# Kernel optimization log

Hardware: AMD Instinct MI355X
Metric: run time of the kernel (lower is better)

## Reference

```python
import jax, jax.numpy as jnp
import numpy as np

S = 14
B = 2
C = 20
LAMBDA_COORD = 5.0
LAMBDA_NOOBJ = 0.5
BATCH = 4096


def setup_inputs() -> dict:
    key = jax.random.key(0)
    k1, k2, k3 = jax.random.split(key, 3)
    pred = jax.random.uniform(k1, (BATCH, S, S, B * 5 + C), dtype=jnp.float32)
    target = jax.random.uniform(k2, (BATCH, S, S, B * 5 + C), dtype=jnp.float32)
    obj = (jax.random.uniform(k3, (BATCH, S, S), dtype=jnp.float32) < 0.15).astype(jnp.float32)
    target = target.at[..., 4].set(obj)
    target = target.at[..., 9].set(obj)
    return {"pred": pred, "target": target}


def _iou(box1, box2):
    # box1, box2: (..., 4) = [x, y, w, h]; elementwise IoU over leading dims
    b1x1 = box1[..., 0] - box1[..., 2] / 2
    b1y1 = box1[..., 1] - box1[..., 3] / 2
    b1x2 = box1[..., 0] + box1[..., 2] / 2
    b1y2 = box1[..., 1] + box1[..., 3] / 2
    b2x1 = box2[..., 0] - box2[..., 2] / 2
    b2y1 = box2[..., 1] - box2[..., 3] / 2
    b2x2 = box2[..., 0] + box2[..., 2] / 2
    b2y2 = box2[..., 1] + box2[..., 3] / 2
    iw = jnp.clip(jnp.minimum(b1x2, b2x2) - jnp.maximum(b1x1, b2x1), 0)
    ih = jnp.clip(jnp.minimum(b1y2, b2y2) - jnp.maximum(b1y1, b2y1), 0)
    inter = iw * ih
    a1 = (b1x2 - b1x1) * (b1y2 - b1y1)
    a2 = (b2x2 - b2x1) * (b2y2 - b2y1)
    return inter / (a1 + a2 - inter + 1e-6)


def reference(pred, target):
    bs = pred.shape[0]
    tb = target[..., : B * 5].reshape(bs, S, S, B, 5)
    pb = pred[..., : B * 5].reshape(bs, S, S, B, 5)
    tcls = target[..., B * 5 :]
    pcls = pred[..., B * 5 :]

    obj_mask = tb[..., 4] > 0          # (bs,S,S,B)
    has_obj = obj_mask[..., 0]         # (bs,S,S)
    noobj_mask = ~obj_mask

    # no-object confidence loss over every non-obj box slot
    conf_err2 = (pb[..., 4] - tb[..., 4]) ** 2
    noobj_loss = jnp.sum(jnp.where(noobj_mask, conf_err2, 0.0))

    # per-box IoU between i-th pred box and i-th target box in each cell
    ious = _iou(pb[..., :4], tb[..., :4])            # (bs,S,S,B)
    best_idx = jnp.argmax(ious, axis=-1)             # (bs,S,S)
    idx = best_idx[..., None, None]
    p_best = jnp.take_along_axis(pb, idx, axis=3)[..., 0, :]  # (bs,S,S,5)
    t_best = jnp.take_along_axis(tb, idx, axis=3)[..., 0, :]

    m = has_obj                                       # (bs,S,S) bool
    mf = m.astype(pred.dtype)

    xy_loss = jnp.sum(mf[..., None] * (p_best[..., :2] - t_best[..., :2]) ** 2)
    p_wh = jnp.sqrt(jnp.abs(p_best[..., 2:4]) + 1e-6)
    t_wh_safe = jnp.where(m[..., None], t_best[..., 2:4], 1.0)  # avoid sqrt(0) grad NaN
    t_wh = jnp.sqrt(t_wh_safe)
    wh_loss = jnp.sum(mf[..., None] * (p_wh - t_wh) ** 2)
    coord_loss = xy_loss + wh_loss

    obj_loss = jnp.sum(mf * (p_best[..., 4] - t_best[..., 4]) ** 2)

    # non-best box confidence pushed to 0 (B=2: the other slot)
    nonbest_conf = jnp.sum(pb[..., 4], axis=-1) - p_best[..., 4]
    noobj_loss = noobj_loss + LAMBDA_NOOBJ * jnp.sum(mf * nonbest_conf ** 2)

    class_loss = jnp.sum(mf[..., None] * (pcls - tcls) ** 2)

    total = LAMBDA_COORD * coord_loss + obj_loss + LAMBDA_NOOBJ * noobj_loss + class_loss
    return total / bs
```

## Files before the change

### kernel.cpp

```cpp
#include <hip/hip_runtime.h>


#define FEAT 30
#define CELLS 802816
#define TILE_CELLS 64
#define TILE_FLOATS (TILE_CELLS * FEAT)
#define BUF_FLOATS (2 * TILE_FLOATS)
#define TILES_PER_BLOCK 8
#define NB (CELLS / (TILE_CELLS * TILES_PER_BLOCK))

__device__ __forceinline__ void load16(const float* g, float* l) {
    __builtin_amdgcn_global_load_lds(
        (const __attribute__((address_space(1))) void*)g,
        (__attribute__((address_space(3))) void*)l, 16, 0, 0);
}

__device__ __forceinline__ float iou_f(float x1, float y1, float w1, float h1,
                                       float x2, float y2, float w2, float h2) {
    float b1x1 = x1 - 0.5f * w1, b1x2 = x1 + 0.5f * w1;
    float b1y1 = y1 - 0.5f * h1, b1y2 = y1 + 0.5f * h1;
    float b2x1 = x2 - 0.5f * w2, b2x2 = x2 + 0.5f * w2;
    float b2y1 = y2 - 0.5f * h2, b2y2 = y2 + 0.5f * h2;
    float iw = fmaxf(fminf(b1x2, b2x2) - fmaxf(b1x1, b2x1), 0.0f);
    float ih = fmaxf(fminf(b1y2, b2y2) - fmaxf(b1y1, b2y1), 0.0f);
    float inter = iw * ih;
    float a1 = (b1x2 - b1x1) * (b1y2 - b1y1);
    float a2 = (b2x2 - b2x1) * (b2y2 - b2y1);
    return inter / (a1 + a2 - inter + 1e-6f);
}

__device__ __forceinline__ float cell_loss(const float* p, const float* t) {
    const bool obj0 = t[4] > 0.0f;
    const bool obj1 = t[9] > 0.0f;
    const float mf = obj0 ? 1.0f : 0.0f;

    float d0 = p[4] - t[4];
    float d1 = p[9] - t[9];
    float noobj = (obj0 ? 0.0f : d0 * d0) + (obj1 ? 0.0f : d1 * d1);

    float iou0 = iou_f(p[0], p[1], p[2], p[3], t[0], t[1], t[2], t[3]);
    float iou1 = iou_f(p[5], p[6], p[7], p[8], t[5], t[6], t[7], t[8]);
    const bool sel1 = iou1 > iou0;

    float pbx = sel1 ? p[5] : p[0];
    float pby = sel1 ? p[6] : p[1];
    float pbw = sel1 ? p[7] : p[2];
    float pbh = sel1 ? p[8] : p[3];
    float pbc = sel1 ? p[9] : p[4];
    float tbx = sel1 ? t[5] : t[0];
    float tby = sel1 ? t[6] : t[1];
    float tbw = sel1 ? t[7] : t[2];
    float tbh = sel1 ? t[8] : t[3];
    float tbc = sel1 ? t[9] : t[4];

    float dx = pbx - tbx, dy = pby - tby;
    float xy = dx * dx + dy * dy;

    float pw = sqrtf(fabsf(pbw) + 1e-6f);
    float ph = sqrtf(fabsf(pbh) + 1e-6f);
    float tw = sqrtf(obj0 ? tbw : 1.0f);
    float th = sqrtf(obj0 ? tbh : 1.0f);
    float dw = pw - tw, dh = ph - th;
    float wh = dw * dw + dh * dh;

    float dc = pbc - tbc;
    float obj_l = dc * dc;

    float nonbest = (p[4] + p[9]) - pbc;
    noobj += 0.5f * mf * nonbest * nonbest;

    float cls = 0.0f;
#pragma unroll
    for (int k = 10; k < FEAT; ++k) {
        float d = p[k] - t[k];
        cls += d * d;
    }

    return 5.0f * mf * (xy + wh) + mf * obj_l + 0.5f * noobj + mf * cls;
}

__global__ __launch_bounds__(64, 2) void yolo_kernel(
        const float* __restrict__ pred, const float* __restrict__ tgt,
        float* __restrict__ out) {
    __shared__ float lds[2 * BUF_FLOATS];

    const int lane = threadIdx.x;
    const float* predT = pred + (long long)blockIdx.x * TILES_PER_BLOCK * TILE_FLOATS;
    const float* tgtT  = tgt  + (long long)blockIdx.x * TILES_PER_BLOCK * TILE_FLOATS;

    const float* pl = predT + lane * 4;
    const float* ml = (lane < 32) ? (predT + 1792 + lane * 4)
                                  : (tgtT - 128 + lane * 4);
    const float* tl = tgtT + 128 + lane * 4;

    auto stage = [&](int buf, int tileFloatOff) {
        float* L = lds + buf * BUF_FLOATS;
        const float* p = pl + tileFloatOff;
        const float* m = ml + tileFloatOff;
        const float* t = tl + tileFloatOff;
#pragma unroll
        for (int j = 0; j < 7; ++j) load16(p + j * 256, L + j * 256);
        load16(m, L + 1792);
#pragma unroll
        for (int j = 0; j < 7; ++j) load16(t + j * 256, L + 2048 + j * 256);
    };

    stage(0, 0);
    float acc = 0.0f;

#pragma unroll 1
    for (int i = 0; i < TILES_PER_BLOCK; ++i) {
        if (i + 1 < TILES_PER_BLOCK) stage((i + 1) & 1, (i + 1) * TILE_FLOATS);

        const float2* pc = (const float2*)(lds + (i & 1) * BUF_FLOATS + lane * FEAT);
        const float2* tc = (const float2*)(lds + (i & 1) * BUF_FLOATS + TILE_FLOATS + lane * FEAT);
        float pf[FEAT], tf[FEAT];
#pragma unroll
        for (int k = 0; k < FEAT / 2; ++k) {
            float2 a = pc[k]; pf[2 * k] = a.x; pf[2 * k + 1] = a.y;
            float2 b = tc[k]; tf[2 * k] = b.x; tf[2 * k + 1] = b.y;
        }
        acc += cell_loss(pf, tf);
    }

    float v = acc;
#pragma unroll
    for (int off = 32; off > 0; off >>= 1) v += __shfl_down(v, off, 64);
    if (lane == 0) atomicAdd(out, v * (1.0f / 4096.0f));
}

extern "C" void kernel_launch(void* const* d_in, const int* in_sizes, int n_in,
                              void* d_out, int out_size, void* d_ws, size_t ws_size,
                              hipStream_t stream) {
    const float* pred = (const float*)d_in[0];
    const float* tgt  = (const float*)d_in[1];
    float* out = (float*)d_out;

    hipMemsetAsync(out, 0, sizeof(float), stream);
    yolo_kernel<<<NB, 64, 0, stream>>>(pred, tgt, out);
}
```

Before: 215.2 us.

## Use one tile per block with partial sums and a separate reduction kernel

Each block now processes a single 64-cell tile, dropping the 8-tile double-buffered loop, so the grid holds 12544 single-wave blocks instead of 1568. Per-block sums go to a workspace array and a second single-block kernel reduces them, replacing the global atomicAdd and the memset. This aims for more memory-level parallelism and less atomic contention. The cost is an extra kernel launch, the loss of load/compute overlap inside a block, and a small serial reduction over 12544 partials.

```diff
diff --git a/kernel.cpp b/kernel.cpp
--- a/kernel.cpp
+++ b/kernel.cpp
@@ -5,9 +5,8 @@
 #define CELLS 802816
 #define TILE_CELLS 64
 #define TILE_FLOATS (TILE_CELLS * FEAT)
-#define BUF_FLOATS (2 * TILE_FLOATS)
-#define TILES_PER_BLOCK 8
-#define NB (CELLS / (TILE_CELLS * TILES_PER_BLOCK))
+#define NB (CELLS / TILE_CELLS)
+#define RED_TPB 256
 
 __device__ __forceinline__ void load16(const float* g, float* l) {
     __builtin_amdgcn_global_load_lds(
@@ -79,54 +78,56 @@
     return 5.0f * mf * (xy + wh) + mf * obj_l + 0.5f * noobj + mf * cls;
 }
 
-__global__ __launch_bounds__(64, 2) void yolo_kernel(
+__global__ __launch_bounds__(64) void yolo_kernel(
         const float* __restrict__ pred, const float* __restrict__ tgt,
-        float* __restrict__ out) {
-    __shared__ float lds[2 * BUF_FLOATS];
+        float* __restrict__ partials) {
+    __shared__ float lds[2 * TILE_FLOATS];
 
     const int lane = threadIdx.x;
-    const float* predT = pred + (long long)blockIdx.x * TILES_PER_BLOCK * TILE_FLOATS;
-    const float* tgtT  = tgt  + (long long)blockIdx.x * TILES_PER_BLOCK * TILE_FLOATS;
+    const float* predT = pred + (long long)blockIdx.x * TILE_FLOATS;
+    const float* tgtT  = tgt  + (long long)blockIdx.x * TILE_FLOATS;
 
     const float* pl = predT + lane * 4;
     const float* ml = (lane < 32) ? (predT + 1792 + lane * 4)
                                   : (tgtT - 128 + lane * 4);
     const float* tl = tgtT + 128 + lane * 4;
+#pragma unroll
+    for (int j = 0; j < 7; ++j) load16(pl + j * 256, lds + j * 256);
+    load16(ml, lds + 1792);
+#pragma unroll
+    for (int j = 0; j < 7; ++j) load16(tl + j * 256, lds + 2048 + j * 256);
 
-    auto stage = [&](int buf, int tileFloatOff) {
-        float* L = lds + buf * BUF_FLOATS;
-        const float* p = pl + tileFloatOff;
-        const float* m = ml + tileFloatOff;
-        const float* t = tl + tileFloatOff;
+    __builtin_amdgcn_s_waitcnt(0x3f70);
+
+    const float2* pc = (const float2*)(lds + lane * FEAT);
+    const float2* tc = (const float2*)(lds + TILE_FLOATS + lane * FEAT);
+    float pf[FEAT], tf[FEAT];
 #pragma unroll
-        for (int j = 0; j < 7; ++j) load16(p + j * 256, L + j * 256);
-        load16(m, L + 1792);
-#pragma unroll
-        for (int j = 0; j < 7; ++j) load16(t + j * 256, L + 2048 + j * 256);
-    };
-
-    stage(0, 0);
-    float acc = 0.0f;
-
-#pragma unroll 1
-    for (int i = 0; i < TILES_PER_BLOCK; ++i) {
-        if (i + 1 < TILES_PER_BLOCK) stage((i + 1) & 1, (i + 1) * TILE_FLOATS);
-
-        const float2* pc = (const float2*)(lds + (i & 1) * BUF_FLOATS + lane * FEAT);
-        const float2* tc = (const float2*)(lds + (i & 1) * BUF_FLOATS + TILE_FLOATS + lane * FEAT);
-        float pf[FEAT], tf[FEAT];
-#pragma unroll
-        for (int k = 0; k < FEAT / 2; ++k) {
-            float2 a = pc[k]; pf[2 * k] = a.x; pf[2 * k + 1] = a.y;
-            float2 b = tc[k]; tf[2 * k] = b.x; tf[2 * k + 1] = b.y;
-        }
-        acc += cell_loss(pf, tf);
+    for (int k = 0; k < FEAT / 2; ++k) {
+        float2 a = pc[k]; pf[2 * k] = a.x; pf[2 * k + 1] = a.y;
+        float2 b = tc[k]; tf[2 * k] = b.x; tf[2 * k + 1] = b.y;
     }
 
-    float v = acc;
+    float v = cell_loss(pf, tf);
 #pragma unroll
     for (int off = 32; off > 0; off >>= 1) v += __shfl_down(v, off, 64);
-    if (lane == 0) atomicAdd(out, v * (1.0f / 4096.0f));
+    if (lane == 0) partials[blockIdx.x] = v;
+}
+
+__global__ __launch_bounds__(RED_TPB) void yolo_reduce_kernel(
+        const float* __restrict__ partials, float* __restrict__ out) {
+    __shared__ float wave_sum[RED_TPB / 64];
+    const int tid = threadIdx.x;
+    float v = 0.0f;
+#pragma unroll 1
+    for (int i = tid; i < NB; i += RED_TPB) v += partials[i];
+#pragma unroll
+    for (int off = 32; off > 0; off >>= 1) v += __shfl_down(v, off, 64);
+    if ((tid & 63) == 0) wave_sum[tid >> 6] = v;
+    __syncthreads();
+    if (tid == 0)
+        out[0] = (wave_sum[0] + wave_sum[1] + wave_sum[2] + wave_sum[3]) *
+                 (1.0f / 4096.0f);
 }
 
 extern "C" void kernel_launch(void* const* d_in, const int* in_sizes, int n_in,
@@ -135,7 +136,8 @@
     const float* pred = (const float*)d_in[0];
     const float* tgt  = (const float*)d_in[1];
     float* out = (float*)d_out;
+    float* partials = (float*)d_ws;
 
-    hipMemsetAsync(out, 0, sizeof(float), stream);
-    yolo_kernel<<<NB, 64, 0, stream>>>(pred, tgt, out);
+    yolo_kernel<<<NB, 64, 0, stream>>>(pred, tgt, partials);
+    yolo_reduce_kernel<<<1, RED_TPB, 0, stream>>>(partials, out);
 }
```

After: 212.9 us. About the same (-1.1%).
